# Kernel optimization log

Hardware: AMD Instinct MI355X
Metric: run time of the kernel (lower is better)

Reference implementation:

```python
import jax, jax.numpy as jnp
import numpy as np

B, L, D, H, W = 2, 1024, 1024, 16, 64  # batch, length, dim, num_head, band_width
DH = D // H  # head_dim = 64


def setup_inputs() -> dict:
    key = jax.random.key(0)
    ks = jax.random.split(key, 7)
    scale = 0.02
    return {
        "x": jax.random.normal(ks[0], (B, L, D), dtype=jnp.float32),
        "Wq": jax.random.normal(ks[1], (D, D), dtype=jnp.float32) * scale,
        "Wk": jax.random.normal(ks[2], (D, D), dtype=jnp.float32) * scale,
        "Wv": jax.random.normal(ks[3], (D, D), dtype=jnp.float32) * scale,
        "Wo": jax.random.normal(ks[4], (D, D), dtype=jnp.float32) * scale,
        "last_k_init": jax.random.normal(ks[5], (W - 1, H, DH), dtype=jnp.float32),
        "last_v_init": jax.random.normal(ks[6], (W - 1, H, DH), dtype=jnp.float32),
    }


def reference(x, Wq, Wk, Wv, Wo, last_k_init, last_v_init):
    b, l, d = x.shape
    w1, h, dh = last_k_init.shape  # band_width-1, num_head, head_dim
    w = w1 + 1

    # torch nn.Linear: y = x @ W.T (no bias)
    q = (x @ Wq.T).reshape(b, l, h, dh)
    k = (x @ Wk.T).reshape(b, l, h, dh)
    v = (x @ Wv.T).reshape(b, l, h, dh)

    # prepend learned initial cache (fresh state: last_k is None)
    last_k = jnp.broadcast_to(last_k_init[None], (b, w1, h, dh))
    last_v = jnp.broadcast_to(last_v_init[None], (b, w1, h, dh))
    k_pad = jnp.concatenate([last_k, k], axis=1)  # [b, l+w-1, h, dh]
    v_pad = jnp.concatenate([last_v, v], axis=1)

    # query at position t attends offsets i in [0, w): key index t + i in padded
    # array == original position t - (w-1) + i  (causal sliding window of width w)
    idx = jnp.arange(l)[:, None] + jnp.arange(w)[None, :]  # [l, w]
    k_win = k_pad[:, idx]  # [b, l, w, h, dh]
    v_win = v_pad[:, idx]  # [b, l, w, h, dh]

    scores = jnp.einsum('blhd,blwhd->blwh', q, k_win) * (dh ** -0.5)
    attn = jax.nn.softmax(scores, axis=2)  # softmax over band offsets
    out = jnp.einsum('blwh,blwhd->blhd', attn, v_win).reshape(b, l, d)
    return out @ Wo.T
```

## Files before the change

### kernel.cpp

```cpp
#include <hip/hip_runtime.h>
#include <hip/hip_bf16.h>
#include <stdint.h>

#define B_ 2
#define L_ 1024
#define D_ 1024
#define H_ 16
#define W_ 64
#define DH_ 64

typedef __attribute__((ext_vector_type(8))) __bf16 bf16x8;
typedef __attribute__((ext_vector_type(4))) float floatx4;

#define AS3(p) ((__attribute__((address_space(3))) void*)(p))
#define AS1(p) ((const __attribute__((address_space(1))) void*)(p))

static __device__ __forceinline__ ushort f2bf(float f) {
    union { float f; uint32_t u; } v{f};
    uint32_t r = v.u + 0x7fff + ((v.u >> 16) & 1);
    return (ushort)(r >> 16);
}
static __device__ __forceinline__ uint32_t pack2(float a, float b) {
    return (uint32_t)f2bf(a) | ((uint32_t)f2bf(b) << 16);
}

__global__ __launch_bounds__(256) void cvt_inputs(
    const float* __restrict__ x, const float* __restrict__ wq, const float* __restrict__ wk,
    const float* __restrict__ wv, const float* __restrict__ wo,
    ushort* __restrict__ xb, ushort* __restrict__ wqb, ushort* __restrict__ wkb,
    ushort* __restrict__ wvb, ushort* __restrict__ wob) {
    const size_t M1 = 1u << 20;
    size_t i4 = ((size_t)blockIdx.x * 256 + threadIdx.x) * 4;
    const float* s; ushort* d; size_t off;
    if (i4 < 2 * M1)      { s = x;  d = xb;  off = i4; }
    else if (i4 < 3 * M1) { s = wq; d = wqb; off = i4 - 2 * M1; }
    else if (i4 < 4 * M1) { s = wk; d = wkb; off = i4 - 3 * M1; }
    else if (i4 < 5 * M1) { s = wv; d = wvb; off = i4 - 4 * M1; }
    else                  { s = wo; d = wob; off = i4 - 5 * M1; }
    float4 f = *(const float4*)(s + off);
    ushort4 o;
    o.x = f2bf(f.x); o.y = f2bf(f.y); o.z = f2bf(f.z); o.w = f2bf(f.w);
    *(ushort4*)(d + off) = o;
}

#define BK 64

__global__ __launch_bounds__(256) void gemm_qkv(
    const ushort* __restrict__ xb,
    const ushort* __restrict__ wqb, const ushort* __restrict__ wkb, const ushort* __restrict__ wvb,
    ushort* __restrict__ q, ushort* __restrict__ k, ushort* __restrict__ v) {
    __shared__ __align__(16) ushort As[128 * BK];
    __shared__ __align__(16) ushort Bs[128 * BK];
    const int tid = threadIdx.x;
    const int m0 = blockIdx.x * 128;
    const int nt = blockIdx.y;
    const int which = nt >> 3;
    const int n0 = (nt & 7) * 128;
    const ushort* wsel = which == 0 ? wqb : (which == 1 ? wkb : wvb);
    ushort* dsel = which == 0 ? q : (which == 1 ? k : v);

    const int lane = tid & 63;
    const int wv_ = tid >> 6;
    const int wm = (wv_ & 1) * 64;
    const int wn = (wv_ >> 1) * 64;
    const int lr = lane & 15;
    const int quad = lane >> 4;

    floatx4 acc[4][4];
#pragma unroll
    for (int i = 0; i < 4; ++i)
#pragma unroll
        for (int j = 0; j < 4; ++j) acc[i][j] = (floatx4){0.f, 0.f, 0.f, 0.f};

    int offA[4], offB[4];
#pragma unroll
    for (int it = 0; it < 4; ++it) {
        int c = tid + it * 256;
        int r = c >> 3, s = c & 7, g = s ^ (r & 7);
        offA[it] = (m0 + r) * 1024 + g * 8;
        offB[it] = (n0 + r) * 1024 + g * 8;
    }

    for (int k0 = 0; k0 < 1024; k0 += BK) {
#pragma unroll
        for (int it = 0; it < 4; ++it)
            __builtin_amdgcn_global_load_lds(AS1(xb + offA[it] + k0), AS3(As + (it * 256 + tid) * 8), 16, 0, 0);
#pragma unroll
        for (int it = 0; it < 4; ++it)
            __builtin_amdgcn_global_load_lds(AS1(wsel + offB[it] + k0), AS3(Bs + (it * 256 + tid) * 8), 16, 0, 0);
        __syncthreads();
#pragma unroll
        for (int ks = 0; ks < 2; ++ks) {
            bf16x8 af[4], bfr[4];
#pragma unroll
            for (int i = 0; i < 4; ++i) {
                int r = wm + i * 16 + lr;
                af[i] = *(const bf16x8*)(As + r * BK + (((ks * 4 + quad) ^ (r & 7)) * 8));
            }
#pragma unroll
            for (int j = 0; j < 4; ++j) {
                int r = wn + j * 16 + lr;
                bfr[j] = *(const bf16x8*)(Bs + r * BK + (((ks * 4 + quad) ^ (r & 7)) * 8));
            }
#pragma unroll
            for (int i = 0; i < 4; ++i)
#pragma unroll
                for (int j = 0; j < 4; ++j)
                    acc[i][j] = __builtin_amdgcn_mfma_f32_16x16x32_bf16(af[i], bfr[j], acc[i][j], 0, 0, 0);
        }
        __syncthreads();
    }

#pragma unroll
    for (int i = 0; i < 4; ++i) {
        int rbase = m0 + wm + i * 16 + quad * 4;
#pragma unroll
        for (int j = 0; j < 4; ++j) {
            int c = n0 + wn + j * 16 + lr;
            int h = c >> 6, dh = c & 63;
#pragma unroll
            for (int r = 0; r < 4; ++r) {
                int m = rbase + r;
                int bb = m >> 10, l = m & 1023;
                dsel[(((size_t)bb * 16 + h) * 1024 + l) * 64 + dh] = f2bf(acc[i][j][r]);
            }
        }
    }
}

__global__ __launch_bounds__(256) void gemm_wo(
    const ushort* __restrict__ ab,
    const ushort* __restrict__ wob,
    float* __restrict__ out) {
    __shared__ __align__(16) ushort As[128 * BK];
    __shared__ __align__(16) ushort Bs[64 * BK];
    const int tid = threadIdx.x;
    const int m0 = blockIdx.x * 128;
    const int n0 = blockIdx.y * 64;
    const int lane = tid & 63;
    const int wv_ = tid >> 6;
    const int wm = (wv_ & 1) * 64;
    const int wn = (wv_ >> 1) * 32;
    const int lr = lane & 15;
    const int quad = lane >> 4;

    floatx4 acc[4][2];
#pragma unroll
    for (int i = 0; i < 4; ++i)
#pragma unroll
        for (int j = 0; j < 2; ++j) acc[i][j] = (floatx4){0.f, 0.f, 0.f, 0.f};

    int offA[4], offB[2];
#pragma unroll
    for (int it = 0; it < 4; ++it) {
        int c = tid + it * 256;
        int r = c >> 3, s = c & 7, g = s ^ (r & 7);
        offA[it] = (m0 + r) * 1024 + g * 8;
    }
#pragma unroll
    for (int it = 0; it < 2; ++it) {
        int c = tid + it * 256;
        int r = c >> 3, s = c & 7, g = s ^ (r & 7);
        offB[it] = (n0 + r) * 1024 + g * 8;
    }

    for (int k0 = 0; k0 < 1024; k0 += BK) {
#pragma unroll
        for (int it = 0; it < 4; ++it)
            __builtin_amdgcn_global_load_lds(AS1(ab + offA[it] + k0), AS3(As + (it * 256 + tid) * 8), 16, 0, 0);
#pragma unroll
        for (int it = 0; it < 2; ++it)
            __builtin_amdgcn_global_load_lds(AS1(wob + offB[it] + k0), AS3(Bs + (it * 256 + tid) * 8), 16, 0, 0);
        __syncthreads();
#pragma unroll
        for (int ks = 0; ks < 2; ++ks) {
            bf16x8 af[4], bfr[2];
#pragma unroll
            for (int i = 0; i < 4; ++i) {
                int r = wm + i * 16 + lr;
                af[i] = *(const bf16x8*)(As + r * BK + (((ks * 4 + quad) ^ (r & 7)) * 8));
            }
#pragma unroll
            for (int j = 0; j < 2; ++j) {
                int r = wn + j * 16 + lr;
                bfr[j] = *(const bf16x8*)(Bs + r * BK + (((ks * 4 + quad) ^ (r & 7)) * 8));
            }
#pragma unroll
            for (int i = 0; i < 4; ++i)
#pragma unroll
                for (int j = 0; j < 2; ++j)
                    acc[i][j] = __builtin_amdgcn_mfma_f32_16x16x32_bf16(af[i], bfr[j], acc[i][j], 0, 0, 0);
        }
        __syncthreads();
    }

#pragma unroll
    for (int i = 0; i < 4; ++i) {
        int rbase = m0 + wm + i * 16 + quad * 4;
#pragma unroll
        for (int j = 0; j < 2; ++j) {
            int c = n0 + wn + j * 16 + lr;
#pragma unroll
            for (int r = 0; r < 4; ++r)
                out[(size_t)(rbase + r) * 1024 + c] = acc[i][j][r];
        }
    }
}

#define STRQ 72
#define STRV 136

__global__ __launch_bounds__(256) void band_attn3(
    const ushort* __restrict__ q,
    const ushort* __restrict__ k,
    const ushort* __restrict__ v,
    const float* __restrict__ lastk,
    const float* __restrict__ lastv,
    ushort* __restrict__ ao) {
    __shared__ __align__(16) ushort Qs[64 * STRQ];
    __shared__ __align__(16) ushort Kw[128 * STRQ];
    __shared__ __align__(16) ushort Vt[64 * STRV];
    __shared__ __align__(16) ushort Ps[64 * STRV];
    const int tid = threadIdx.x;
    const int lane = tid & 63;
    const int wid = tid >> 6;
    const int l0 = blockIdx.x * 64;
    const int b = blockIdx.y >> 4, h = blockIdx.y & 15;
    const size_t hb = (size_t)(b * 16 + h) * 1024 * 64;

#pragma unroll
    for (int it = 0; it < 2; ++it) {
        int c = tid + it * 256;
        int rr = c >> 3, cc = (c & 7) * 8;
        *(uint4*)(Qs + rr * STRQ + cc) = *(const uint4*)(q + hb + (size_t)(l0 + rr) * 64 + cc);
    }
#pragma unroll
    for (int it = 0; it < 4; ++it) {
        int c = tid + it * 256;
        int j = c >> 3, cc = (c & 7) * 8;
        int pos = l0 + j - 63;
        uint4 t = {0u, 0u, 0u, 0u};
        if (j < 127) {
            if (pos >= 0) {
                t = *(const uint4*)(k + hb + (size_t)pos * 64 + cc);
            } else {
                const float* sk = lastk + ((size_t)j * 16 + h) * 64 + cc;
                float4 a0 = *(const float4*)sk, a1 = *(const float4*)(sk + 4);
                t.x = pack2(a0.x, a0.y); t.y = pack2(a0.z, a0.w);
                t.z = pack2(a1.x, a1.y); t.w = pack2(a1.z, a1.w);
            }
        }
        *(uint4*)(Kw + j * STRQ + cc) = t;
    }
#pragma unroll
    for (int it = 0; it < 4; ++it) {
        int c = tid + it * 256;
        int j = c >> 3, d8 = (c & 7) * 8;
        int pos = l0 + j - 63;
        ushort tv[8];
        if (j >= 127) {
#pragma unroll
            for (int t = 0; t < 8; ++t) tv[t] = 0;
        } else if (pos >= 0) {
            union { uint4 u4; ushort us[8]; } tu;
            tu.u4 = *(const uint4*)(v + hb + (size_t)pos * 64 + d8);
#pragma unroll
            for (int t = 0; t < 8; ++t) tv[t] = tu.us[t];
        } else {
            const float* sv = lastv + ((size_t)j * 16 + h) * 64 + d8;
#pragma unroll
            for (int t = 0; t < 8; ++t) tv[t] = f2bf(sv[t]);
        }
#pragma unroll
        for (int t = 0; t < 8; ++t) Vt[(size_t)(d8 + t) * STRV + j] = tv[t];
    }
    __syncthreads();

    const int lr = lane & 15;
    const int quad = lane >> 4;

    floatx4 sa[8];
#pragma unroll
    for (int nt = 0; nt < 8; ++nt) sa[nt] = (floatx4){0.f, 0.f, 0.f, 0.f};
    bf16x8 aq[2];
#pragma unroll
    for (int ks = 0; ks < 2; ++ks)
        aq[ks] = *(const bf16x8*)(Qs + (wid * 16 + lr) * STRQ + ks * 32 + quad * 8);
#pragma unroll
    for (int ks = 0; ks < 2; ++ks)
#pragma unroll
        for (int nt = 0; nt < 8; ++nt) {
            bf16x8 bk = *(const bf16x8*)(Kw + (nt * 16 + lr) * STRQ + ks * 32 + quad * 8);
            sa[nt] = __builtin_amdgcn_mfma_f32_16x16x32_bf16(aq[ks], bk, sa[nt], 0, 0, 0);
        }

#pragma unroll
    for (int rr = 0; rr < 4; ++rr) {
        int i_loc = wid * 16 + quad * 4 + rr;
        float sv[8];
        float mv = -1e30f;
#pragma unroll
        for (int nt = 0; nt < 8; ++nt) {
            int j = nt * 16 + lr;
            int w = j - i_loc;
            sv[nt] = (w >= 0 && w < 64) ? sa[nt][rr] * 0.125f : -1e30f;
            mv = fmaxf(mv, sv[nt]);
        }
#pragma unroll
        for (int off = 8; off; off >>= 1) mv = fmaxf(mv, __shfl_xor(mv, off, 16));
        float sum = 0.f;
#pragma unroll
        for (int nt = 0; nt < 8; ++nt) {
            sv[nt] = __expf(sv[nt] - mv);
            sum += sv[nt];
        }
#pragma unroll
        for (int off = 8; off; off >>= 1) sum += __shfl_xor(sum, off, 16);
        float inv = 1.f / sum;
#pragma unroll
        for (int nt = 0; nt < 8; ++nt)
            Ps[(size_t)i_loc * STRV + nt * 16 + lr] = f2bf(sv[nt] * inv);
    }

    floatx4 oa[4];
#pragma unroll
    for (int nt = 0; nt < 4; ++nt) oa[nt] = (floatx4){0.f, 0.f, 0.f, 0.f};
#pragma unroll
    for (int ks = 0; ks < 4; ++ks) {
        bf16x8 ap = *(const bf16x8*)(Ps + (wid * 16 + lr) * STRV + ks * 32 + quad * 8);
#pragma unroll
        for (int nt = 0; nt < 4; ++nt) {
            bf16x8 bv = *(const bf16x8*)(Vt + (nt * 16 + lr) * STRV + ks * 32 + quad * 8);
            oa[nt] = __builtin_amdgcn_mfma_f32_16x16x32_bf16(ap, bv, oa[nt], 0, 0, 0);
        }
    }

#pragma unroll
    for (int nt = 0; nt < 4; ++nt) {
        int d = nt * 16 + lr;
#pragma unroll
        for (int rr = 0; rr < 4; ++rr) {
            int i_loc = wid * 16 + quad * 4 + rr;
            ao[((size_t)b * 1024 + l0 + i_loc) * 1024 + h * 64 + d] = f2bf(oa[nt][rr]);
        }
    }
}

extern "C" void kernel_launch(void* const* d_in, const int* in_sizes, int n_in,
                              void* d_out, int out_size, void* d_ws, size_t ws_size,
                              hipStream_t stream) {
    const float* x     = (const float*)d_in[0];
    const float* Wq    = (const float*)d_in[1];
    const float* Wk    = (const float*)d_in[2];
    const float* Wv    = (const float*)d_in[3];
    const float* Wo    = (const float*)d_in[4];
    const float* lastk = (const float*)d_in[5];
    const float* lastv = (const float*)d_in[6];
    float* out = (float*)d_out;

    const size_t M1 = 1u << 20;
    ushort* xb  = (ushort*)d_ws;
    ushort* wqb = xb + 2 * M1;
    ushort* wkb = wqb + M1;
    ushort* wvb = wkb + M1;
    ushort* wob = wvb + M1;
    ushort* qh  = wob + M1;
    ushort* kh  = qh + 2 * M1;
    ushort* vh  = kh + 2 * M1;
    ushort* ao  = vh + 2 * M1;

    cvt_inputs<<<6144, 256, 0, stream>>>(x, Wq, Wk, Wv, Wo, xb, wqb, wkb, wvb, wob);
    gemm_qkv<<<dim3(16, 24), 256, 0, stream>>>(xb, wqb, wkb, wvb, qh, kh, vh);
    band_attn3<<<dim3(16, 32), 256, 0, stream>>>(qh, kh, vh, lastk, lastv, ao);
    gemm_wo<<<dim3(16, 16), 256, 0, stream>>>(ao, wob, out);
}
```

Before: 128.4 us.

## Register-prefetch next K tile in QKV and output GEMMs

```diff
diff --git a/kernel.cpp b/kernel.cpp
--- a/kernel.cpp
+++ b/kernel.cpp
@@ -81,14 +81,28 @@
         offB[it] = (n0 + r) * 1024 + g * 8;
     }
 
+    uint4 ra[4], rb[4];
+#pragma unroll
+    for (int it = 0; it < 4; ++it) {
+        ra[it] = *(const uint4*)(xb + offA[it]);
+        rb[it] = *(const uint4*)(wsel + offB[it]);
+    }
+#pragma unroll
+    for (int it = 0; it < 4; ++it) {
+        *(uint4*)(As + (it * 256 + tid) * 8) = ra[it];
+        *(uint4*)(Bs + (it * 256 + tid) * 8) = rb[it];
+    }
+    __syncthreads();
+
     for (int k0 = 0; k0 < 1024; k0 += BK) {
-#pragma unroll
-        for (int it = 0; it < 4; ++it)
-            __builtin_amdgcn_global_load_lds(AS1(xb + offA[it] + k0), AS3(As + (it * 256 + tid) * 8), 16, 0, 0);
-#pragma unroll
-        for (int it = 0; it < 4; ++it)
-            __builtin_amdgcn_global_load_lds(AS1(wsel + offB[it] + k0), AS3(Bs + (it * 256 + tid) * 8), 16, 0, 0);
-        __syncthreads();
+        const bool more = (k0 + BK) < 1024;
+        if (more) {
+#pragma unroll
+            for (int it = 0; it < 4; ++it) {
+                ra[it] = *(const uint4*)(xb + offA[it] + k0 + BK);
+                rb[it] = *(const uint4*)(wsel + offB[it] + k0 + BK);
+            }
+        }
 #pragma unroll
         for (int ks = 0; ks < 2; ++ks) {
             bf16x8 af[4], bfr[4];
@@ -107,6 +121,14 @@
 #pragma unroll
                 for (int j = 0; j < 4; ++j)
                     acc[i][j] = __builtin_amdgcn_mfma_f32_16x16x32_bf16(af[i], bfr[j], acc[i][j], 0, 0, 0);
+        }
+        __syncthreads();
+        if (more) {
+#pragma unroll
+            for (int it = 0; it < 4; ++it) {
+                *(uint4*)(As + (it * 256 + tid) * 8) = ra[it];
+                *(uint4*)(Bs + (it * 256 + tid) * 8) = rb[it];
+            }
         }
         __syncthreads();
     }
@@ -164,14 +186,25 @@
         offB[it] = (n0 + r) * 1024 + g * 8;
     }
 
+    uint4 ra[4], rb[2];
+#pragma unroll
+    for (int it = 0; it < 4; ++it) ra[it] = *(const uint4*)(ab + offA[it]);
+#pragma unroll
+    for (int it = 0; it < 2; ++it) rb[it] = *(const uint4*)(wob + offB[it]);
+#pragma unroll
+    for (int it = 0; it < 4; ++it) *(uint4*)(As + (it * 256 + tid) * 8) = ra[it];
+#pragma unroll
+    for (int it = 0; it < 2; ++it) *(uint4*)(Bs + (it * 256 + tid) * 8) = rb[it];
+    __syncthreads();
+
     for (int k0 = 0; k0 < 1024; k0 += BK) {
-#pragma unroll
-        for (int it = 0; it < 4; ++it)
-            __builtin_amdgcn_global_load_lds(AS1(ab + offA[it] + k0), AS3(As + (it * 256 + tid) * 8), 16, 0, 0);
-#pragma unroll
-        for (int it = 0; it < 2; ++it)
-            __builtin_amdgcn_global_load_lds(AS1(wob + offB[it] + k0), AS3(Bs + (it * 256 + tid) * 8), 16, 0, 0);
-        __syncthreads();
+        const bool more = (k0 + BK) < 1024;
+        if (more) {
+#pragma unroll
+            for (int it = 0; it < 4; ++it) ra[it] = *(const uint4*)(ab + offA[it] + k0 + BK);
+#pragma unroll
+            for (int it = 0; it < 2; ++it) rb[it] = *(const uint4*)(wob + offB[it] + k0 + BK);
+        }
 #pragma unroll
         for (int ks = 0; ks < 2; ++ks) {
             bf16x8 af[4], bfr[2];
@@ -190,6 +223,13 @@
 #pragma unroll
                 for (int j = 0; j < 2; ++j)
                     acc[i][j] = __builtin_amdgcn_mfma_f32_16x16x32_bf16(af[i], bfr[j], acc[i][j], 0, 0, 0);
+        }
+        __syncthreads();
+        if (more) {
+#pragma unroll
+            for (int it = 0; it < 4; ++it) *(uint4*)(As + (it * 256 + tid) * 8) = ra[it];
+#pragma unroll
+            for (int it = 0; it < 2; ++it) *(uint4*)(Bs + (it * 256 + tid) * 8) = rb[it];
         }
         __syncthreads();
     }
```

Result: slower. 197.1 us (+53.5%).
